# Kernel tuning notes

Measured on AMD Instinct MI355X. Metric: run time of the kernel, lower is better.

## Reference

```python
import jax, jax.numpy as jnp
import numpy as np

CUTOFF = 5.0
LOG2 = 0.6931471805599453

def ssp(x):
    # ShiftedSoftplus: softplus(x) - log(2)
    return jax.nn.softplus(x) - LOG2

def setup_inputs() -> dict:
    key = jax.random.key(0)
    ks = jax.random.split(key, 10)
    B, P, A, G, F, E = 2, 4096, 96, 1, 32, 20
    return {
        "scalar": jax.random.normal(ks[0], (B, A, G, F), jnp.float32),
        "scalar_reciever": jax.random.normal(ks[1], (B, P, G, F), jnp.float32),
        "expansion": jax.random.uniform(ks[2], (B, P, A, E), jnp.float32),
        "mask": jax.random.uniform(ks[3], (B, P, A, G), jnp.float32),
        "edge_distance": jax.random.uniform(ks[4], (B, P, A, 1), jnp.float32) * CUTOFF,
        "W1e": jax.random.normal(ks[5], (E, F), jnp.float32) * 0.1,
        "b1e": jnp.zeros((F,), jnp.float32),
        "W2e": jax.random.normal(ks[6], (F, F), jnp.float32) * 0.1,
        "b2e": jnp.zeros((F,), jnp.float32),
        "W1n": jax.random.normal(ks[7], (2 * F, F), jnp.float32) * 0.1,
        "b1n": jnp.zeros((F,), jnp.float32),
        "W2n": jax.random.normal(ks[8], (F, F), jnp.float32) * 0.1,
        "b2n": jnp.zeros((F,), jnp.float32),
    }

def reference(scalar, scalar_reciever, expansion, mask, edge_distance,
              W1e, b1e, W2e, b2e, W1n, b1n, W2n, b2n):
    F = scalar.shape[-1]
    # edge gate: 2-layer MLP on expansion, times soft cutoff  -> [B,P,A,F]
    gates = ssp(expansion @ W1e + b1e) @ W2e + b2e
    gates = gates * (1.0 - jax.nn.sigmoid(5.0 * (edge_distance - (CUTOFF - 1.5))))
    # pairwise node MLP: split first linear into source/target halves instead of
    # materializing the [B,P,A,G,2F] repeat+concat tensor (same math).
    Ws, Wt = W1n[:F], W1n[F:]
    src = jnp.einsum('bagf,fh->bagh', scalar, Ws)            # [B,A,G,H]
    tgt = jnp.einsum('bpgf,fh->bpgh', scalar_reciever, Wt)   # [B,P,G,H]
    h = src[:, None, :, :, :] + tgt[:, :, None, :, :] + b1n  # [B,P,A,G,H]
    nodes = ssp(h) @ W2n + b2n                               # [B,P,A,G,F]
    result = mask[..., None] * (gates[..., None, :] * nodes)
    return jnp.sum(result, axis=-3)                          # sum over atoms A -> [B,P,G,F]

if __name__ == "__main__":
    out = reference(**setup_inputs())
    print(out.shape)
```

## Files before the change

### kernel.cpp

```cpp
#include <hip/hip_runtime.h>

#define NB   2
#define NP   4096
#define NA   96
#define NF   32
#define NE   20
#define NBP  (NB*NP)

typedef __attribute__((ext_vector_type(8)))  short bf16x8;
typedef __attribute__((ext_vector_type(16))) float f32x16;

union Frag { bf16x8 v; int i[4]; };

__device__ __forceinline__ int cvtpk(float lo, float hi) {
  int r;
  asm("v_cvt_pk_bf16_f32 %0, %1, %2" : "=v"(r) : "v"(lo), "v"(hi));
  return r;
}
__device__ __forceinline__ float ssp_f(float x) {
  float t = __expf(-fabsf(x));
  return fmaxf(x, 0.0f) + __logf(1.0f + t) - 0.69314718056f;
}
__device__ __forceinline__ f32x16 mfma32(const Frag a, const Frag b, f32x16 c) {
  return __builtin_amdgcn_mfma_f32_32x32x16_bf16(a.v, b.v, c, 0, 0, 0);
}
__device__ __forceinline__ f32x16 ld_bias16(const float* __restrict__ base ) {
  const float4* p = reinterpret_cast<const float4*>(base);
  float4 q0 = p[0], q1 = p[2], q2 = p[4], q3 = p[6];
  f32x16 c;
  c[0]=q0.x;  c[1]=q0.y;  c[2]=q0.z;  c[3]=q0.w;
  c[4]=q1.x;  c[5]=q1.y;  c[6]=q1.z;  c[7]=q1.w;
  c[8]=q2.x;  c[9]=q2.y;  c[10]=q2.z; c[11]=q2.w;
  c[12]=q3.x; c[13]=q3.y; c[14]=q3.z; c[15]=q3.w;
  return c;
}
__device__ __forceinline__ Frag ld_frag(const int4* __restrict__ p) {
  int4 q = *p;
  Frag f; f.i[0] = q.x; f.i[1] = q.y; f.i[2] = q.z; f.i[3] = q.w;
  return f;
}

__global__ __launch_bounds__(256)
void prep_kernel(const float* __restrict__ scalar,
                 const float* __restrict__ sr,
                 const float* __restrict__ W1e,
                 const float* __restrict__ W2e,
                 const float* __restrict__ W2n,
                 const float* __restrict__ W1n,
                 const float* __restrict__ b1n,
                 float* __restrict__ tgt_ws,
                 float* __restrict__ src_ws,
                 int4* __restrict__ ftab)
{
  const int blk = blockIdx.x;
  if (blk < 1048) {
    int i = blk * 256 + threadIdx.x;
    int f   = i & 31;
    int row = i >> 5;
    const float* x;
    const float* W;
    float acc;
    if (row < NBP) { x = sr + row * NF;             W = W1n + NF * NF; acc = 0.0f;   }
    else           { x = scalar + (row - NBP) * NF; W = W1n;           acc = b1n[f]; }
    float4 xv[8];
#pragma unroll
    for (int q = 0; q < 8; ++q) xv[q] = reinterpret_cast<const float4*>(x)[q];
#pragma unroll
    for (int q = 0; q < 8; ++q) {
      acc = fmaf(xv[q].x, W[(4 * q + 0) * NF + f], acc);
      acc = fmaf(xv[q].y, W[(4 * q + 1) * NF + f], acc);
      acc = fmaf(xv[q].z, W[(4 * q + 2) * NF + f], acc);
      acc = fmaf(xv[q].w, W[(4 * q + 3) * NF + f], acc);
    }
    if (row < NBP) tgt_ws[i] = acc;
    else           src_ws[(row - NBP) * NF + f] = acc;
  } else {
    int e = (blk - 1048) * 256 + threadIdx.x;
    if (e < 384) {
      const int f  = e >> 6;
      const int l  = e & 63;
      const int c  = l & 31;
      const int hw = l >> 5;
      const float* W = (f < 2) ? W1e : ((f < 4) ? W2e : W2n);
      const int kbase = (f & 1) ? (16 + 8 * hw) : (8 * hw);
      int4 v;
      int* vi = reinterpret_cast<int*>(&v);
#pragma unroll
      for (int r = 0; r < 4; ++r) {
        int ka = kbase + 2 * r, kb = ka + 1;
        bool pa = (f == 1) && (ka >= NE);
        bool pb = (f == 1) && (kb >= NE);
        float lo = W[(pa ? 0 : ka) * NF + c]; lo = pa ? 0.0f : lo;
        float hi = W[(pb ? 0 : kb) * NF + c]; hi = pb ? 0.0f : hi;
        vi[r] = cvtpk(lo, hi);
      }
      ftab[e] = v;
    }
  }
}

__global__ __launch_bounds__(256, 4)
void fused_t(const float* __restrict__ expansion,
             const float* __restrict__ mask,
             const float* __restrict__ edge_dist,
             const float* __restrict__ b1e,
             const float* __restrict__ b2e,
             const float* __restrict__ b2n,
             const float* __restrict__ src_ws,
             const float* __restrict__ tgt_ws,
             const int4* __restrict__ ftab,
             float* __restrict__ out)
{
  const int tid  = threadIdx.x;
  const int wid  = tid >> 6;
  const int lane = tid & 63;
  const int col  = lane & 31;
  const int hw   = lane >> 5;

  const unsigned w  = blockIdx.x * 4 + wid;
  const unsigned bp = w / 3u;
  const int      t  = (int)(w - 3u * bp);
  const int      b  = (int)(bp >> 12);
  const int      a  = t * 32 + col;

  Frag aw1a = ld_frag(ftab + 0 * 64 + lane);
  Frag aw1b = ld_frag(ftab + 1 * 64 + lane);
  Frag aw2a = ld_frag(ftab + 2 * 64 + lane);
  Frag aw2b = ld_frag(ftab + 3 * 64 + lane);
  Frag aw3a = ld_frag(ftab + 4 * 64 + lane);
  Frag aw3b = ld_frag(ftab + 5 * 64 + lane);
  const float mk = mask[bp * NA + a];
  const float dd = edge_dist[bp * NA + a];
  const float be = b2e[col];
  const float bn = b2n[col];

  const float* ea = expansion + (size_t)bp * (NA * NE) + a * NE;
  float4 e0 = *reinterpret_cast<const float4*>(ea + 8 * hw);
  float4 e1 = *reinterpret_cast<const float4*>(ea + 8 * hw + 4);
  float4 e2 = *reinterpret_cast<const float4*>(ea + 16);

  const float z  = __expf(5.0f * (dd - 3.5f));
  const float em = mk * __builtin_amdgcn_rcpf(1.0f + z);

  Frag b1f0, b1f1;
  b1f0.i[0] = cvtpk(e0.x, e0.y);
  b1f0.i[1] = cvtpk(e0.z, e0.w);
  b1f0.i[2] = cvtpk(e1.x, e1.y);
  b1f0.i[3] = cvtpk(e1.z, e1.w);
  b1f1.i[0] = hw ? 0 : cvtpk(e2.x, e2.y);
  b1f1.i[1] = hw ? 0 : cvtpk(e2.z, e2.w);
  b1f1.i[2] = 0;
  b1f1.i[3] = 0;

  f32x16 d1 = ld_bias16(b1e + 4 * hw);
  d1 = mfma32(aw1a, b1f0, d1);
  d1 = mfma32(aw1b, b1f1, d1);
#pragma unroll
  for (int r = 0; r < 16; ++r) d1[r] = ssp_f(d1[r]);

  int u0 = cvtpk(d1[0],  d1[1]);
  int u1 = cvtpk(d1[2],  d1[3]);
  int u2 = cvtpk(d1[4],  d1[5]);
  int u3 = cvtpk(d1[6],  d1[7]);
  int u4 = cvtpk(d1[8],  d1[9]);
  int u5 = cvtpk(d1[10], d1[11]);
  int u6 = cvtpk(d1[12], d1[13]);
  int u7 = cvtpk(d1[14], d1[15]);
  asm("v_permlane32_swap_b32 %0, %1" : "+v"(u0), "+v"(u2));
  asm("v_permlane32_swap_b32 %0, %1" : "+v"(u1), "+v"(u3));
  asm("v_permlane32_swap_b32 %0, %1" : "+v"(u4), "+v"(u6));
  asm("v_permlane32_swap_b32 %0, %1" : "+v"(u5), "+v"(u7));
  Frag b2f0, b2f1;
  b2f0.i[0] = u0; b2f0.i[1] = u1; b2f0.i[2] = u2; b2f0.i[3] = u3;
  b2f1.i[0] = u4; b2f1.i[1] = u5; b2f1.i[2] = u6; b2f1.i[3] = u7;

  f32x16 d2;
#pragma unroll
  for (int r = 0; r < 16; ++r) d2[r] = be;
  d2 = mfma32(b2f0, aw2a, d2);
  d2 = mfma32(b2f1, aw2b, d2);

  const float* sa = src_ws + (b * NA + a) * NF;
  const float* tg = tgt_ws + bp * NF;
  float4 s0 = *reinterpret_cast<const float4*>(sa + 8 * hw);
  float4 s1 = *reinterpret_cast<const float4*>(sa + 8 * hw + 4);
  float4 s2 = *reinterpret_cast<const float4*>(sa + 16 + 8 * hw);
  float4 s3 = *reinterpret_cast<const float4*>(sa + 16 + 8 * hw + 4);
  float4 t0 = *reinterpret_cast<const float4*>(tg + 8 * hw);
  float4 t1 = *reinterpret_cast<const float4*>(tg + 8 * hw + 4);
  float4 t2 = *reinterpret_cast<const float4*>(tg + 16 + 8 * hw);
  float4 t3 = *reinterpret_cast<const float4*>(tg + 16 + 8 * hw + 4);
  Frag b3f0, b3f1;
  b3f0.i[0] = cvtpk(em * ssp_f(s0.x + t0.x), em * ssp_f(s0.y + t0.y));
  b3f0.i[1] = cvtpk(em * ssp_f(s0.z + t0.z), em * ssp_f(s0.w + t0.w));
  b3f0.i[2] = cvtpk(em * ssp_f(s1.x + t1.x), em * ssp_f(s1.y + t1.y));
  b3f0.i[3] = cvtpk(em * ssp_f(s1.z + t1.z), em * ssp_f(s1.w + t1.w));
  b3f1.i[0] = cvtpk(em * ssp_f(s2.x + t2.x), em * ssp_f(s2.y + t2.y));
  b3f1.i[1] = cvtpk(em * ssp_f(s2.z + t2.z), em * ssp_f(s2.w + t2.w));
  b3f1.i[2] = cvtpk(em * ssp_f(s3.x + t3.x), em * ssp_f(s3.y + t3.y));
  b3f1.i[3] = cvtpk(em * ssp_f(s3.z + t3.z), em * ssp_f(s3.w + t3.w));

  f32x16 d3;
#pragma unroll
  for (int r = 0; r < 16; ++r) d3[r] = bn;
  d3 = mfma32(b3f0, aw3a, d3);
  d3 = mfma32(b3f1, aw3b, d3);

  int p0 = cvtpk(d2[0]  * d3[0],  d2[1]  * d3[1]);
  int p1 = cvtpk(d2[2]  * d3[2],  d2[3]  * d3[3]);
  int p2 = cvtpk(d2[4]  * d3[4],  d2[5]  * d3[5]);
  int p3 = cvtpk(d2[6]  * d3[6],  d2[7]  * d3[7]);
  int p4 = cvtpk(d2[8]  * d3[8],  d2[9]  * d3[9]);
  int p5 = cvtpk(d2[10] * d3[10], d2[11] * d3[11]);
  int p6 = cvtpk(d2[12] * d3[12], d2[13] * d3[13]);
  int p7 = cvtpk(d2[14] * d3[14], d2[15] * d3[15]);
  asm("v_permlane32_swap_b32 %0, %1" : "+v"(p0), "+v"(p2));
  asm("v_permlane32_swap_b32 %0, %1" : "+v"(p1), "+v"(p3));
  asm("v_permlane32_swap_b32 %0, %1" : "+v"(p4), "+v"(p6));
  asm("v_permlane32_swap_b32 %0, %1" : "+v"(p5), "+v"(p7));
  Frag pb0, pb1;
  pb0.i[0] = p0; pb0.i[1] = p1; pb0.i[2] = p2; pb0.i[3] = p3;
  pb1.i[0] = p4; pb1.i[1] = p5; pb1.i[2] = p6; pb1.i[3] = p7;

  Frag aones;
  aones.i[0] = 0x3F803F80; aones.i[1] = 0x3F803F80;
  aones.i[2] = 0x3F803F80; aones.i[3] = 0x3F803F80;
  f32x16 red;
#pragma unroll
  for (int r = 0; r < 16; ++r) red[r] = 0.0f;
  red = mfma32(aones, pb0, red);
  red = mfma32(aones, pb1, red);

  if (lane < 32) atomicAdd(out + bp * NF + lane, red[0]);
}

extern "C" void kernel_launch(void* const* d_in, const int* in_sizes, int n_in,
                              void* d_out, int out_size, void* d_ws, size_t ws_size,
                              hipStream_t stream) {
  const float* scalar    = (const float*)d_in[0];
  const float* sreciever = (const float*)d_in[1];
  const float* expansion = (const float*)d_in[2];
  const float* maskp     = (const float*)d_in[3];
  const float* edist     = (const float*)d_in[4];
  const float* W1e       = (const float*)d_in[5];
  const float* b1e       = (const float*)d_in[6];
  const float* W2e       = (const float*)d_in[7];
  const float* b2e       = (const float*)d_in[8];
  const float* W1n       = (const float*)d_in[9];
  const float* b1n       = (const float*)d_in[10];
  const float* W2n       = (const float*)d_in[11];
  const float* b2n       = (const float*)d_in[12];
  float* out    = (float*)d_out;
  float* src_ws = (float*)d_ws;
  int4*  ftab   = (int4*)((char*)d_ws + 24576);
  float* tgt_ws = (float*)((char*)d_ws + 24576 + 6144);

  hipMemsetAsync(out, 0, (size_t)out_size * sizeof(float), stream);
  prep_kernel<<<1050, 256, 0, stream>>>(scalar, sreciever, W1e, W2e, W2n,
                                        W1n, b1n, tgt_ws, src_ws, ftab);
  fused_t<<<6144, 256, 0, stream>>>(expansion, maskp, edist,
                                    b1e, b2e, b2n, src_ws, tgt_ws, ftab, out);
}
```

Measured before the change: 145.8 us.

## Loop each wave over all atom tiles, accumulate in registers, drop atomics and memset

Each wave now handles one (b,p) pair and loops over the three 32-atom tiles, accumulating the reduction in the MFMA accumulator. The result is then written directly, with no atomicAdd and no memset of the output. Grid size drops threefold and the launch bound asks for 8 waves per SIMD so occupancy can hide latency. Weight fragments are reloaded inside the loop to save registers, which adds repeated loads. The loop also serializes work within each wave.

```diff
diff --git a/kernel.cpp b/kernel.cpp
--- a/kernel.cpp
+++ b/kernel.cpp
@@ -99,7 +99,7 @@
   }
 }
 
-__global__ __launch_bounds__(256, 4)
+__global__ __launch_bounds__(256, 8)
 void fused_t(const float* __restrict__ expansion,
              const float* __restrict__ mask,
              const float* __restrict__ edge_dist,
@@ -117,121 +117,122 @@
   const int col  = lane & 31;
   const int hw   = lane >> 5;
 
-  const unsigned w  = blockIdx.x * 4 + wid;
-  const unsigned bp = w / 3u;
-  const int      t  = (int)(w - 3u * bp);
-  const int      b  = (int)(bp >> 12);
-  const int      a  = t * 32 + col;
-
-  Frag aw1a = ld_frag(ftab + 0 * 64 + lane);
-  Frag aw1b = ld_frag(ftab + 1 * 64 + lane);
-  Frag aw2a = ld_frag(ftab + 2 * 64 + lane);
-  Frag aw2b = ld_frag(ftab + 3 * 64 + lane);
-  Frag aw3a = ld_frag(ftab + 4 * 64 + lane);
-  Frag aw3b = ld_frag(ftab + 5 * 64 + lane);
-  const float mk = mask[bp * NA + a];
-  const float dd = edge_dist[bp * NA + a];
-  const float be = b2e[col];
-  const float bn = b2n[col];
-
-  const float* ea = expansion + (size_t)bp * (NA * NE) + a * NE;
-  float4 e0 = *reinterpret_cast<const float4*>(ea + 8 * hw);
-  float4 e1 = *reinterpret_cast<const float4*>(ea + 8 * hw + 4);
-  float4 e2 = *reinterpret_cast<const float4*>(ea + 16);
-
-  const float z  = __expf(5.0f * (dd - 3.5f));
-  const float em = mk * __builtin_amdgcn_rcpf(1.0f + z);
-
-  Frag b1f0, b1f1;
-  b1f0.i[0] = cvtpk(e0.x, e0.y);
-  b1f0.i[1] = cvtpk(e0.z, e0.w);
-  b1f0.i[2] = cvtpk(e1.x, e1.y);
-  b1f0.i[3] = cvtpk(e1.z, e1.w);
-  b1f1.i[0] = hw ? 0 : cvtpk(e2.x, e2.y);
-  b1f1.i[1] = hw ? 0 : cvtpk(e2.z, e2.w);
-  b1f1.i[2] = 0;
-  b1f1.i[3] = 0;
-
-  f32x16 d1 = ld_bias16(b1e + 4 * hw);
-  d1 = mfma32(aw1a, b1f0, d1);
-  d1 = mfma32(aw1b, b1f1, d1);
-#pragma unroll
-  for (int r = 0; r < 16; ++r) d1[r] = ssp_f(d1[r]);
-
-  int u0 = cvtpk(d1[0],  d1[1]);
-  int u1 = cvtpk(d1[2],  d1[3]);
-  int u2 = cvtpk(d1[4],  d1[5]);
-  int u3 = cvtpk(d1[6],  d1[7]);
-  int u4 = cvtpk(d1[8],  d1[9]);
-  int u5 = cvtpk(d1[10], d1[11]);
-  int u6 = cvtpk(d1[12], d1[13]);
-  int u7 = cvtpk(d1[14], d1[15]);
-  asm("v_permlane32_swap_b32 %0, %1" : "+v"(u0), "+v"(u2));
-  asm("v_permlane32_swap_b32 %0, %1" : "+v"(u1), "+v"(u3));
-  asm("v_permlane32_swap_b32 %0, %1" : "+v"(u4), "+v"(u6));
-  asm("v_permlane32_swap_b32 %0, %1" : "+v"(u5), "+v"(u7));
-  Frag b2f0, b2f1;
-  b2f0.i[0] = u0; b2f0.i[1] = u1; b2f0.i[2] = u2; b2f0.i[3] = u3;
-  b2f1.i[0] = u4; b2f1.i[1] = u5; b2f1.i[2] = u6; b2f1.i[3] = u7;
-
-  f32x16 d2;
-#pragma unroll
-  for (int r = 0; r < 16; ++r) d2[r] = be;
-  d2 = mfma32(b2f0, aw2a, d2);
-  d2 = mfma32(b2f1, aw2b, d2);
-
-  const float* sa = src_ws + (b * NA + a) * NF;
-  const float* tg = tgt_ws + bp * NF;
-  float4 s0 = *reinterpret_cast<const float4*>(sa + 8 * hw);
-  float4 s1 = *reinterpret_cast<const float4*>(sa + 8 * hw + 4);
-  float4 s2 = *reinterpret_cast<const float4*>(sa + 16 + 8 * hw);
-  float4 s3 = *reinterpret_cast<const float4*>(sa + 16 + 8 * hw + 4);
-  float4 t0 = *reinterpret_cast<const float4*>(tg + 8 * hw);
-  float4 t1 = *reinterpret_cast<const float4*>(tg + 8 * hw + 4);
-  float4 t2 = *reinterpret_cast<const float4*>(tg + 16 + 8 * hw);
-  float4 t3 = *reinterpret_cast<const float4*>(tg + 16 + 8 * hw + 4);
-  Frag b3f0, b3f1;
-  b3f0.i[0] = cvtpk(em * ssp_f(s0.x + t0.x), em * ssp_f(s0.y + t0.y));
-  b3f0.i[1] = cvtpk(em * ssp_f(s0.z + t0.z), em * ssp_f(s0.w + t0.w));
-  b3f0.i[2] = cvtpk(em * ssp_f(s1.x + t1.x), em * ssp_f(s1.y + t1.y));
-  b3f0.i[3] = cvtpk(em * ssp_f(s1.z + t1.z), em * ssp_f(s1.w + t1.w));
-  b3f1.i[0] = cvtpk(em * ssp_f(s2.x + t2.x), em * ssp_f(s2.y + t2.y));
-  b3f1.i[1] = cvtpk(em * ssp_f(s2.z + t2.z), em * ssp_f(s2.w + t2.w));
-  b3f1.i[2] = cvtpk(em * ssp_f(s3.x + t3.x), em * ssp_f(s3.y + t3.y));
-  b3f1.i[3] = cvtpk(em * ssp_f(s3.z + t3.z), em * ssp_f(s3.w + t3.w));
-
-  f32x16 d3;
-#pragma unroll
-  for (int r = 0; r < 16; ++r) d3[r] = bn;
-  d3 = mfma32(b3f0, aw3a, d3);
-  d3 = mfma32(b3f1, aw3b, d3);
-
-  int p0 = cvtpk(d2[0]  * d3[0],  d2[1]  * d3[1]);
-  int p1 = cvtpk(d2[2]  * d3[2],  d2[3]  * d3[3]);
-  int p2 = cvtpk(d2[4]  * d3[4],  d2[5]  * d3[5]);
-  int p3 = cvtpk(d2[6]  * d3[6],  d2[7]  * d3[7]);
-  int p4 = cvtpk(d2[8]  * d3[8],  d2[9]  * d3[9]);
-  int p5 = cvtpk(d2[10] * d3[10], d2[11] * d3[11]);
-  int p6 = cvtpk(d2[12] * d3[12], d2[13] * d3[13]);
-  int p7 = cvtpk(d2[14] * d3[14], d2[15] * d3[15]);
-  asm("v_permlane32_swap_b32 %0, %1" : "+v"(p0), "+v"(p2));
-  asm("v_permlane32_swap_b32 %0, %1" : "+v"(p1), "+v"(p3));
-  asm("v_permlane32_swap_b32 %0, %1" : "+v"(p4), "+v"(p6));
-  asm("v_permlane32_swap_b32 %0, %1" : "+v"(p5), "+v"(p7));
-  Frag pb0, pb1;
-  pb0.i[0] = p0; pb0.i[1] = p1; pb0.i[2] = p2; pb0.i[3] = p3;
-  pb1.i[0] = p4; pb1.i[1] = p5; pb1.i[2] = p6; pb1.i[3] = p7;
-
-  Frag aones;
-  aones.i[0] = 0x3F803F80; aones.i[1] = 0x3F803F80;
-  aones.i[2] = 0x3F803F80; aones.i[3] = 0x3F803F80;
+  const int bp = blockIdx.x * 4 + wid;
+  const int b  = bp >> 12;
+
+  const float* expb  = expansion + (size_t)bp * (NA * NE);
+  const float* maskb = mask      + bp * NA;
+  const float* distb = edge_dist + bp * NA;
+  const float* srcb  = src_ws    + b * (NA * NF);
+  const float* tg    = tgt_ws    + bp * NF;
+  const float  be    = b2e[col];
+  const float  bn    = b2n[col];
+
   f32x16 red;
 #pragma unroll
   for (int r = 0; r < 16; ++r) red[r] = 0.0f;
-  red = mfma32(aones, pb0, red);
-  red = mfma32(aones, pb1, red);
-
-  if (lane < 32) atomicAdd(out + bp * NF + lane, red[0]);
+
+#pragma unroll 1
+  for (int t = 0; t < 3; ++t) {
+    const int a = t * 32 + col;
+
+    const float* ea = expb + a * NE;
+    float4 e0 = *reinterpret_cast<const float4*>(ea + 8 * hw);
+    float4 e1 = *reinterpret_cast<const float4*>(ea + 8 * hw + 4);
+    float4 e2 = *reinterpret_cast<const float4*>(ea + 16);
+    const float mk = maskb[a];
+    const float dd = distb[a];
+
+    const float z  = __expf(5.0f * (dd - 3.5f));
+    const float em = mk * __builtin_amdgcn_rcpf(1.0f + z);
+
+    Frag b1f0, b1f1;
+    b1f0.i[0] = cvtpk(e0.x, e0.y);
+    b1f0.i[1] = cvtpk(e0.z, e0.w);
+    b1f0.i[2] = cvtpk(e1.x, e1.y);
+    b1f0.i[3] = cvtpk(e1.z, e1.w);
+    b1f1.i[0] = hw ? 0 : cvtpk(e2.x, e2.y);
+    b1f1.i[1] = hw ? 0 : cvtpk(e2.z, e2.w);
+    b1f1.i[2] = 0;
+    b1f1.i[3] = 0;
+
+    f32x16 d1 = ld_bias16(b1e + 4 * hw);
+    d1 = mfma32(ld_frag(ftab + 0 * 64 + lane), b1f0, d1);
+    d1 = mfma32(ld_frag(ftab + 1 * 64 + lane), b1f1, d1);
+#pragma unroll
+    for (int r = 0; r < 16; ++r) d1[r] = ssp_f(d1[r]);
+
+    int u0 = cvtpk(d1[0],  d1[1]);
+    int u1 = cvtpk(d1[2],  d1[3]);
+    int u2 = cvtpk(d1[4],  d1[5]);
+    int u3 = cvtpk(d1[6],  d1[7]);
+    int u4 = cvtpk(d1[8],  d1[9]);
+    int u5 = cvtpk(d1[10], d1[11]);
+    int u6 = cvtpk(d1[12], d1[13]);
+    int u7 = cvtpk(d1[14], d1[15]);
+    asm("v_permlane32_swap_b32 %0, %1" : "+v"(u0), "+v"(u2));
+    asm("v_permlane32_swap_b32 %0, %1" : "+v"(u1), "+v"(u3));
+    asm("v_permlane32_swap_b32 %0, %1" : "+v"(u4), "+v"(u6));
+    asm("v_permlane32_swap_b32 %0, %1" : "+v"(u5), "+v"(u7));
+    Frag b2f0, b2f1;
+    b2f0.i[0] = u0; b2f0.i[1] = u1; b2f0.i[2] = u2; b2f0.i[3] = u3;
+    b2f1.i[0] = u4; b2f1.i[1] = u5; b2f1.i[2] = u6; b2f1.i[3] = u7;
+
+    f32x16 d2;
+#pragma unroll
+    for (int r = 0; r < 16; ++r) d2[r] = be;
+    d2 = mfma32(b2f0, ld_frag(ftab + 2 * 64 + lane), d2);
+    d2 = mfma32(b2f1, ld_frag(ftab + 3 * 64 + lane), d2);
+
+    const float* sa = srcb + a * NF;
+    float4 s0 = *reinterpret_cast<const float4*>(sa + 8 * hw);
+    float4 s1 = *reinterpret_cast<const float4*>(sa + 8 * hw + 4);
+    float4 s2 = *reinterpret_cast<const float4*>(sa + 16 + 8 * hw);
+    float4 s3 = *reinterpret_cast<const float4*>(sa + 16 + 8 * hw + 4);
+    float4 t0 = *reinterpret_cast<const float4*>(tg + 8 * hw);
+    float4 t1 = *reinterpret_cast<const float4*>(tg + 8 * hw + 4);
+    float4 t2 = *reinterpret_cast<const float4*>(tg + 16 + 8 * hw);
+    float4 t3 = *reinterpret_cast<const float4*>(tg + 16 + 8 * hw + 4);
+    Frag b3f0, b3f1;
+    b3f0.i[0] = cvtpk(em * ssp_f(s0.x + t0.x), em * ssp_f(s0.y + t0.y));
+    b3f0.i[1] = cvtpk(em * ssp_f(s0.z + t0.z), em * ssp_f(s0.w + t0.w));
+    b3f0.i[2] = cvtpk(em * ssp_f(s1.x + t1.x), em * ssp_f(s1.y + t1.y));
+    b3f0.i[3] = cvtpk(em * ssp_f(s1.z + t1.z), em * ssp_f(s1.w + t1.w));
+    b3f1.i[0] = cvtpk(em * ssp_f(s2.x + t2.x), em * ssp_f(s2.y + t2.y));
+    b3f1.i[1] = cvtpk(em * ssp_f(s2.z + t2.z), em * ssp_f(s2.w + t2.w));
+    b3f1.i[2] = cvtpk(em * ssp_f(s3.x + t3.x), em * ssp_f(s3.y + t3.y));
+    b3f1.i[3] = cvtpk(em * ssp_f(s3.z + t3.z), em * ssp_f(s3.w + t3.w));
+
+    f32x16 d3;
+#pragma unroll
+    for (int r = 0; r < 16; ++r) d3[r] = bn;
+    d3 = mfma32(b3f0, ld_frag(ftab + 4 * 64 + lane), d3);
+    d3 = mfma32(b3f1, ld_frag(ftab + 5 * 64 + lane), d3);
+
+    int p0 = cvtpk(d2[0]  * d3[0],  d2[1]  * d3[1]);
+    int p1 = cvtpk(d2[2]  * d3[2],  d2[3]  * d3[3]);
+    int p2 = cvtpk(d2[4]  * d3[4],  d2[5]  * d3[5]);
+    int p3 = cvtpk(d2[6]  * d3[6],  d2[7]  * d3[7]);
+    int p4 = cvtpk(d2[8]  * d3[8],  d2[9]  * d3[9]);
+    int p5 = cvtpk(d2[10] * d3[10], d2[11] * d3[11]);
+    int p6 = cvtpk(d2[12] * d3[12], d2[13] * d3[13]);
+    int p7 = cvtpk(d2[14] * d3[14], d2[15] * d3[15]);
+    asm("v_permlane32_swap_b32 %0, %1" : "+v"(p0), "+v"(p2));
+    asm("v_permlane32_swap_b32 %0, %1" : "+v"(p1), "+v"(p3));
+    asm("v_permlane32_swap_b32 %0, %1" : "+v"(p4), "+v"(p6));
+    asm("v_permlane32_swap_b32 %0, %1" : "+v"(p5), "+v"(p7));
+    Frag pb0, pb1;
+    pb0.i[0] = p0; pb0.i[1] = p1; pb0.i[2] = p2; pb0.i[3] = p3;
+    pb1.i[0] = p4; pb1.i[1] = p5; pb1.i[2] = p6; pb1.i[3] = p7;
+
+    Frag aones;
+    aones.i[0] = 0x3F803F80; aones.i[1] = 0x3F803F80;
+    aones.i[2] = 0x3F803F80; aones.i[3] = 0x3F803F80;
+    red = mfma32(aones, pb0, red);
+    red = mfma32(aones, pb1, red);
+  }
+
+  if (lane < 32) out[bp * NF + lane] = red[0];
 }
 
 extern "C" void kernel_launch(void* const* d_in, const int* in_sizes, int n_in,
@@ -255,9 +256,8 @@
   int4*  ftab   = (int4*)((char*)d_ws + 24576);
   float* tgt_ws = (float*)((char*)d_ws + 24576 + 6144);
 
-  hipMemsetAsync(out, 0, (size_t)out_size * sizeof(float), stream);
   prep_kernel<<<1050, 256, 0, stream>>>(scalar, sreciever, W1e, W2e, W2n,
                                         W1n, b1n, tgt_ws, src_ws, ftab);
-  fused_t<<<6144, 256, 0, stream>>>(expansion, maskp, edist,
-                                    b1e, b2e, b2n, src_ws, tgt_ws, ftab, out);
-}
+  fused_t<<<NBP / 4, 256, 0, stream>>>(expansion, maskp, edist,
+                                       b1e, b2e, b2n, src_ws, tgt_ws, ftab, out);
+}
```

New measurement: 273.1 us. 87.4% more time.
